# Performance work log

Hardware: AMD Instinct MI355X
Metric: run time of the kernel (lower is better)

## Reference

```python
import jax, jax.numpy as jnp
import numpy as np

TEMP = 0.05
EPS = 1e-8  # torch CosineSimilarity eps

def _l2_normalize(x):
    # matches torch: x / max(||x||, eps)
    n = jnp.sqrt(jnp.sum(x * x, axis=-1, keepdims=True))
    return x / jnp.maximum(n, EPS)

def setup_inputs() -> dict:
    key = jax.random.key(0)
    k1, k2, k3 = jax.random.split(key, 3)
    N, D = 8192, 256
    return {
        "anc": jax.random.normal(k1, (N, D), dtype=jnp.float32),
        "pos": jax.random.normal(k2, (N, D), dtype=jnp.float32),
        "neg": jax.random.normal(k3, (N, D), dtype=jnp.float32),
    }

def reference(anc, pos, neg):
    a = _l2_normalize(anc)            # [N, D]
    p = _l2_normalize(pos)            # [N, D]
    n = _l2_normalize(neg)            # [N, D]
    pos_sim = jnp.einsum('id,jd->ij', a, p) / TEMP   # [N, N]
    neg_sim = jnp.einsum('id,jd->ij', a, n) / TEMP   # [N, N]
    logits = jnp.concatenate([pos_sim, neg_sim], axis=1)  # [N, 2N]
    N_ = logits.shape[0]
    logp = jax.nn.log_softmax(logits, axis=-1)
    labels = jnp.arange(N_)
    # CrossEntropyLoss with mean reduction
    return -jnp.mean(logp[labels, labels])
```

## Files before the change

kernel.cpp:

```cpp
#include <hip/hip_runtime.h>
#include <hip/hip_bf16.h>

#define N_ROWS 8192
#define DIM 256
#define TEMP_INV 20.0f
#define C2F 1.7889516e-3f

typedef __attribute__((ext_vector_type(4))) int i32x4;

__global__ void __launch_bounds__(256) prep_kernel(
    const float* __restrict__ anc, const float* __restrict__ pos,
    const float* __restrict__ neg, char* __restrict__ a8,
    char* __restrict__ p8, char* __restrict__ n8,
    float* __restrict__ diag, float* __restrict__ rowsum,
    float* __restrict__ out) {
  __shared__ __align__(16) char t8[8192];
  const int lane = threadIdx.x & 63;
  const int w = threadIdx.x >> 6;

  if (blockIdx.x < 2048) {
    int wid = blockIdx.x * 4 + w;
    float4 a = reinterpret_cast<const float4*>(anc + (size_t)wid * DIM)[lane];
    float4 p = reinterpret_cast<const float4*>(pos + (size_t)wid * DIM)[lane];
    float d  = a.x * p.x + a.y * p.y + a.z * p.z + a.w * p.w;
    float na = a.x * a.x + a.y * a.y + a.z * a.z + a.w * a.w;
    float np = p.x * p.x + p.y * p.y + p.z * p.z + p.w * p.w;
#pragma unroll
    for (int m = 32; m; m >>= 1) {
      d  += __shfl_xor(d, m);
      na += __shfl_xor(na, m);
      np += __shfl_xor(np, m);
    }
    float rna = fmaxf(sqrtf(na), 1e-8f);
    float s = 127.0f / rna;
    int q0 = (int)rintf(a.x * s), q1 = (int)rintf(a.y * s);
    int q2 = (int)rintf(a.z * s), q3 = (int)rintf(a.w * s);
    unsigned pk = (q0 & 0xFF) | ((q1 & 0xFF) << 8) |
                  ((q2 & 0xFF) << 16) | ((q3 & 0xFF) << 24);
    *reinterpret_cast<unsigned*>(a8 + (size_t)wid * DIM + (lane << 2)) = pk;
    if (lane == 0) {
      diag[wid] = TEMP_INV * d / (rna * fmaxf(sqrtf(np), 1e-8f));
      rowsum[wid] = 0.f;
    }
    return;
  }
  const int b = blockIdx.x - 2048;
  if (b == 511 && threadIdx.x == 0) out[0] = 0.f;
  const float* src = (b < 256) ? pos : neg;
  char* dst = (b < 256) ? p8 : n8;
  const int pb = b & 255;
#pragma unroll
  for (int i = 0; i < 8; ++i) {
    int r = i * 4 + w;
    float4 v = reinterpret_cast<const float4*>(src + (size_t)(pb * 32 + r) * DIM)[lane];
    float ss = v.x * v.x + v.y * v.y + v.z * v.z + v.w * v.w;
#pragma unroll
    for (int m = 32; m; m >>= 1) ss += __shfl_xor(ss, m);
    float s = 127.0f / fmaxf(sqrtf(ss), 1e-8f);
    int q0 = (int)rintf(v.x * s), q1 = (int)rintf(v.y * s);
    int q2 = (int)rintf(v.z * s), q3 = (int)rintf(v.w * s);
    unsigned pk = (q0 & 0xFF) | ((q1 & 0xFF) << 8) |
                  ((q2 & 0xFF) << 16) | ((q3 & 0xFF) << 24);
    *reinterpret_cast<unsigned*>(t8 + ((lane >> 2) << 9) + (r << 4) +
                                 ((lane & 3) << 2)) = pk;
  }
  __syncthreads();
  const uint4* ts = reinterpret_cast<const uint4*>(t8);
  uint4* outp = reinterpret_cast<uint4*>(dst + (size_t)pb * 8192);
  outp[threadIdx.x]       = ts[threadIdx.x];
  outp[threadIdx.x + 256] = ts[threadIdx.x + 256];
}

__global__ void __launch_bounds__(256, 4) fused_kernel(
    const char* __restrict__ a8, const char* __restrict__ p8,
    const char* __restrict__ n8, float* __restrict__ rowsum) {
  __shared__ __align__(16) char smem[3 * 8192];
  const int tid  = threadIdx.x;
  const int lane = tid & 63;
  const int w    = tid >> 6;
  const int rb   = blockIdx.x >> 5;
  const int cc   = blockIdx.x & 31;
  const char* B = (cc < 16) ? (p8 + (size_t)cc * 16 * 8192)
                            : (n8 + (size_t)(cc - 16) * 16 * 8192);
  const int row0 = rb * 128 + w * 32;
  const int ar = lane & 15;
  const int g  = lane >> 4;
  const int vbase = (g << 9) + (ar << 4);

  i32x4 af[2][4];
#pragma unroll
  for (int rf = 0; rf < 2; ++rf)
#pragma unroll
    for (int km = 0; km < 4; ++km) {
      af[rf][km] = *reinterpret_cast<const i32x4*>(
          a8 + (size_t)(row0 + rf * 16 + ar) * DIM + km * 64 + g * 16);
      asm volatile("" : "+v"(af[rf][km]));
    }

#define STAGE(slot, p)                                                         \
  {                                                                            \
    _Pragma("unroll")                                                          \
    for (int j = 0; j < 2; ++j) {                                              \
      const int L = (w << 1) | j;                                              \
      const char* src = B + ((size_t)(p) << 13) + (L << 10) + (lane << 4);     \
      char* dst = (char*)smem + ((slot) << 13) + (L << 10);                    \
      __builtin_amdgcn_global_load_lds(                                        \
          (const __attribute__((address_space(1))) void*)src,                  \
          (__attribute__((address_space(3))) void*)dst, 16, 0, 0);             \
    }                                                                          \
  }

#define MMI(A, Bf, C) __builtin_amdgcn_mfma_i32_16x16x64_i8((A), (Bf), (C), 0, 0, 0)

#define CLUSTER(CFOFF)                                                         \
  {                                                                            \
    i32x4 bf[4];                                                               \
    _Pragma("unroll")                                                          \
    for (int km = 0; km < 4; ++km)                                             \
      bf[km] = *reinterpret_cast<const i32x4*>(pbase + (km << 11) + (CFOFF));  \
    i32x4 acc[2];                                                              \
    _Pragma("unroll")                                                          \
    for (int rf = 0; rf < 2; ++rf) acc[rf] = MMI(af[rf][0], bf[0], zeroi);     \
    _Pragma("unroll")                                                          \
    for (int km = 1; km < 4; ++km)                                             \
      _Pragma("unroll")                                                        \
      for (int rf = 0; rf < 2; ++rf)                                           \
        acc[rf] = MMI(af[rf][km], bf[km], acc[rf]);                            \
    _Pragma("unroll")                                                          \
    for (int rf = 0; rf < 2; ++rf)                                             \
      _Pragma("unroll")                                                        \
      for (int q = 0; q < 4; ++q)                                              \
        psum[rf][q] += __builtin_amdgcn_exp2f((float)acc[rf][q] * C2F);        \
  }

  float psum[2][4];
#pragma unroll
  for (int rf = 0; rf < 2; ++rf)
#pragma unroll
    for (int q = 0; q < 4; ++q) psum[rf][q] = 0.f;
  const i32x4 zeroi = {0, 0, 0, 0};

  STAGE(0, 0);
  STAGE(1, 1);
  int rd = 0;
  for (int it = 0; it < 16; ++it) {
    if (it <= 14) asm volatile("s_waitcnt vmcnt(2)" ::: "memory");
    else          asm volatile("s_waitcnt vmcnt(0)" ::: "memory");
    __builtin_amdgcn_s_barrier();
    const char* pbase = smem + (rd << 13) + vbase;
    const int st = (rd == 0) ? 2 : rd - 1;
    CLUSTER(0);
    if (it <= 13) STAGE(st, it + 2);
    CLUSTER(256);
    rd = (rd == 2) ? 0 : rd + 1;
  }

#pragma unroll
  for (int rf = 0; rf < 2; ++rf)
#pragma unroll
    for (int q = 0; q < 4; ++q) {
      float s = psum[rf][q];
      s += __shfl_xor(s, 1);
      s += __shfl_xor(s, 2);
      s += __shfl_xor(s, 4);
      s += __shfl_xor(s, 8);
      if (ar == 0)
        atomicAdd(rowsum + row0 + rf * 16 + g * 4 + q, s);
    }
#undef STAGE
#undef CLUSTER
#undef MMI
}

__global__ void __launch_bounds__(512) loss_kernel(
    const float* __restrict__ rowsum, const float* __restrict__ diag,
    float* __restrict__ out) {
  __shared__ float sh[8];
  int i = blockIdx.x * 512 + threadIdx.x;
  float acc = logf(rowsum[i]) - diag[i];
#pragma unroll
  for (int m = 32; m; m >>= 1) acc += __shfl_xor(acc, m);
  if ((threadIdx.x & 63) == 0) sh[threadIdx.x >> 6] = acc;
  __syncthreads();
  if (threadIdx.x == 0) {
    float t = 0.f;
#pragma unroll
    for (int j = 0; j < 8; ++j) t += sh[j];
    atomicAdd(out, t / (float)N_ROWS);
  }
}

extern "C" void kernel_launch(void* const* d_in, const int* in_sizes, int n_in,
                              void* d_out, int out_size, void* d_ws, size_t ws_size,
                              hipStream_t stream) {
  const float* anc = (const float*)d_in[0];
  const float* pos = (const float*)d_in[1];
  const float* neg = (const float*)d_in[2];
  char* ws = (char*)d_ws;
  char* a8 = ws;
  char* p8 = ws + (size_t)N_ROWS * DIM;
  char* n8 = p8 + (size_t)N_ROWS * DIM;
  float* diag = (float*)(ws + (size_t)3 * N_ROWS * DIM);
  float* rowsum = diag + N_ROWS;
  float* out = (float*)d_out;

  prep_kernel<<<2048 + 512, 256, 0, stream>>>(anc, pos, neg, a8, p8, n8, diag, rowsum, out);
  fused_kernel<<<64 * 32, 256, 0, stream>>>(a8, p8, n8, rowsum);
  loss_kernel<<<16, 512, 0, stream>>>(rowsum, diag, out);
}
```

Measured before the change: 56.89 us.

## Double rows per block and fold loss reduction into fused kernel via tickets

Each wave now holds 64 anchor rows (4 row fragments) instead of 32, so each staged B tile feeds twice as many MFMAs and the grid halves to 1024 blocks. The separate loss kernel is removed: the last block to finish each 256-row band, found through an atomic ticket counter, computes log(rowsum)-diag and adds it to the output. This cuts B-tile traffic and one kernel launch. In exchange it raises register pressure under launch bounds of 4 blocks and adds a threadfence plus atomic tail.

```diff
diff --git a/kernel.cpp b/kernel.cpp
--- a/kernel.cpp
+++ b/kernel.cpp
@@ -13,12 +13,13 @@
     const float* __restrict__ neg, char* __restrict__ a8,
     char* __restrict__ p8, char* __restrict__ n8,
     float* __restrict__ diag, float* __restrict__ rowsum,
-    float* __restrict__ out) {
+    float* __restrict__ out, int* __restrict__ done) {
   __shared__ __align__(16) char t8[8192];
   const int lane = threadIdx.x & 63;
   const int w = threadIdx.x >> 6;
 
   if (blockIdx.x < 2048) {
+    if (blockIdx.x < 32 && threadIdx.x == 0) done[blockIdx.x] = 0;
     int wid = blockIdx.x * 4 + w;
     float4 a = reinterpret_cast<const float4*>(anc + (size_t)wid * DIM)[lane];
     float4 p = reinterpret_cast<const float4*>(pos + (size_t)wid * DIM)[lane];
@@ -73,8 +74,11 @@
 
 __global__ void __launch_bounds__(256, 4) fused_kernel(
     const char* __restrict__ a8, const char* __restrict__ p8,
-    const char* __restrict__ n8, float* __restrict__ rowsum) {
+    const char* __restrict__ n8, float* __restrict__ rowsum,
+    const float* __restrict__ diag, float* __restrict__ out,
+    int* __restrict__ done) {
   __shared__ __align__(16) char smem[3 * 8192];
+  __shared__ int ticket;
   const int tid  = threadIdx.x;
   const int lane = tid & 63;
   const int w    = tid >> 6;
@@ -82,14 +86,14 @@
   const int cc   = blockIdx.x & 31;
   const char* B = (cc < 16) ? (p8 + (size_t)cc * 16 * 8192)
                             : (n8 + (size_t)(cc - 16) * 16 * 8192);
-  const int row0 = rb * 128 + w * 32;
+  const int row0 = rb * 256 + w * 64;
   const int ar = lane & 15;
   const int g  = lane >> 4;
   const int vbase = (g << 9) + (ar << 4);
 
-  i32x4 af[2][4];
-#pragma unroll
-  for (int rf = 0; rf < 2; ++rf)
+  i32x4 af[4][4];
+#pragma unroll
+  for (int rf = 0; rf < 4; ++rf)
 #pragma unroll
     for (int km = 0; km < 4; ++km) {
       af[rf][km] = *reinterpret_cast<const i32x4*>(
@@ -118,24 +122,24 @@
     _Pragma("unroll")                                                          \
     for (int km = 0; km < 4; ++km)                                             \
       bf[km] = *reinterpret_cast<const i32x4*>(pbase + (km << 11) + (CFOFF));  \
-    i32x4 acc[2];                                                              \
-    _Pragma("unroll")                                                          \
-    for (int rf = 0; rf < 2; ++rf) acc[rf] = MMI(af[rf][0], bf[0], zeroi);     \
+    i32x4 acc[4];                                                              \
+    _Pragma("unroll")                                                          \
+    for (int rf = 0; rf < 4; ++rf) acc[rf] = MMI(af[rf][0], bf[0], zeroi);     \
     _Pragma("unroll")                                                          \
     for (int km = 1; km < 4; ++km)                                             \
       _Pragma("unroll")                                                        \
-      for (int rf = 0; rf < 2; ++rf)                                           \
+      for (int rf = 0; rf < 4; ++rf)                                           \
         acc[rf] = MMI(af[rf][km], bf[km], acc[rf]);                            \
     _Pragma("unroll")                                                          \
-    for (int rf = 0; rf < 2; ++rf)                                             \
+    for (int rf = 0; rf < 4; ++rf)                                             \
       _Pragma("unroll")                                                        \
       for (int q = 0; q < 4; ++q)                                              \
         psum[rf][q] += __builtin_amdgcn_exp2f((float)acc[rf][q] * C2F);        \
   }
 
-  float psum[2][4];
-#pragma unroll
-  for (int rf = 0; rf < 2; ++rf)
+  float psum[4][4];
+#pragma unroll
+  for (int rf = 0; rf < 4; ++rf)
 #pragma unroll
     for (int q = 0; q < 4; ++q) psum[rf][q] = 0.f;
   const i32x4 zeroi = {0, 0, 0, 0};
@@ -156,7 +160,7 @@
   }
 
 #pragma unroll
-  for (int rf = 0; rf < 2; ++rf)
+  for (int rf = 0; rf < 4; ++rf)
 #pragma unroll
     for (int q = 0; q < 4; ++q) {
       float s = psum[rf][q];
@@ -167,27 +171,22 @@
       if (ar == 0)
         atomicAdd(rowsum + row0 + rf * 16 + g * 4 + q, s);
     }
+
+  __threadfence();
+  __syncthreads();
+  if (tid == 0) ticket = atomicAdd(&done[rb], 1);
+  __syncthreads();
+  if (ticket == 31) {
+    int r = rb * 256 + tid;
+    float v = atomicAdd(&rowsum[r], 0.0f);
+    float l = logf(v) - diag[r];
+#pragma unroll
+    for (int m = 32; m; m >>= 1) l += __shfl_xor(l, m);
+    if ((tid & 63) == 0) atomicAdd(out, l * (1.0f / (float)N_ROWS));
+  }
 #undef STAGE
 #undef CLUSTER
 #undef MMI
-}
-
-__global__ void __launch_bounds__(512) loss_kernel(
-    const float* __restrict__ rowsum, const float* __restrict__ diag,
-    float* __restrict__ out) {
-  __shared__ float sh[8];
-  int i = blockIdx.x * 512 + threadIdx.x;
-  float acc = logf(rowsum[i]) - diag[i];
-#pragma unroll
-  for (int m = 32; m; m >>= 1) acc += __shfl_xor(acc, m);
-  if ((threadIdx.x & 63) == 0) sh[threadIdx.x >> 6] = acc;
-  __syncthreads();
-  if (threadIdx.x == 0) {
-    float t = 0.f;
-#pragma unroll
-    for (int j = 0; j < 8; ++j) t += sh[j];
-    atomicAdd(out, t / (float)N_ROWS);
-  }
 }
 
 extern "C" void kernel_launch(void* const* d_in, const int* in_sizes, int n_in,
@@ -202,9 +201,9 @@
   char* n8 = p8 + (size_t)N_ROWS * DIM;
   float* diag = (float*)(ws + (size_t)3 * N_ROWS * DIM);
   float* rowsum = diag + N_ROWS;
+  int* done = (int*)(rowsum + N_ROWS);
   float* out = (float*)d_out;
 
-  prep_kernel<<<2048 + 512, 256, 0, stream>>>(anc, pos, neg, a8, p8, n8, diag, rowsum, out);
-  fused_kernel<<<64 * 32, 256, 0, stream>>>(a8, p8, n8, rowsum);
-  loss_kernel<<<16, 512, 0, stream>>>(rowsum, diag, out);
+  prep_kernel<<<2048 + 512, 256, 0, stream>>>(anc, pos, neg, a8, p8, n8, diag, rowsum, out, done);
+  fused_kernel<<<32 * 32, 256, 0, stream>>>(a8, p8, n8, rowsum, diag, out, done);
 }
```

New measurement: 142.8 us. 2.51x slower.
